# Optimization experiments

Hardware: AMD Instinct MI355X
Metric: run time of the kernel (lower is better)

The kernel has to match this reference:

```python
import jax, jax.numpy as jnp
import numpy as np

B, S, D = 2, 2048, 4096
H, KVH, HD = 32, 8, 128
THETA = 10000.0


def setup_inputs() -> dict:
    key = jax.random.key(0)
    k1, k2, k3 = jax.random.split(key, 3)
    hidden_states = jax.random.normal(k1, (B, S, D), jnp.float32)
    w_qkv = jax.random.normal(k2, ((KVH * 2 + H) * HD, D), jnp.float32) * 0.02
    w_dense = jax.random.normal(k3, (D, D), jnp.float32) * 0.02
    return {"hidden_states": hidden_states, "w_qkv": w_qkv, "w_dense": w_dense}


def _rope(x, pos):
    # x: [B, H, S, HD]; Falcon rotary embedding (rotate_half convention)
    inv_freq = 1.0 / (THETA ** (jnp.arange(0, HD, 2, dtype=jnp.float32) / HD))
    freqs = pos[:, None] * inv_freq[None, :]           # [S, HD/2]
    emb = jnp.concatenate([freqs, freqs], axis=-1)      # [S, HD]
    cos, sin = jnp.cos(emb), jnp.sin(emb)
    x1, x2 = x[..., : HD // 2], x[..., HD // 2 :]
    rot = jnp.concatenate([-x2, x1], axis=-1)
    return x * cos + rot * sin


def reference(hidden_states, w_qkv, w_dense):
    # fused QKV projection (FalconLinear, no bias)
    fused = jnp.einsum('bsd,ed->bse', hidden_states, w_qkv)  # [B,S,(2KVH+H)*HD]
    g = H // KVH  # query heads per kv head
    qkv = fused.reshape(B, S, KVH, g + 2, HD)
    q = qkv[:, :, :, :g]                        # [B,S,KVH,g,HD]
    k = jnp.broadcast_to(qkv[:, :, :, g:g + 1], q.shape)
    v = jnp.broadcast_to(qkv[:, :, :, g + 1:g + 2], q.shape)
    q, k, v = (t.reshape(B, S, H, HD).transpose(0, 2, 1, 3) for t in (q, k, v))
    pos = jnp.arange(S, dtype=jnp.float32)
    q = _rope(q, pos)
    k = _rope(k, pos)
    scores = jnp.einsum('bhqd,bhkd->bhqk', q, k) / jnp.sqrt(jnp.float32(HD))
    causal = jnp.tril(jnp.ones((S, S), dtype=bool))
    scores = jnp.where(causal, scores, jnp.float32(-1e9))
    attn = jax.nn.softmax(scores, axis=-1)
    out = jnp.einsum('bhqk,bhkd->bhqd', attn, v)
    out = out.transpose(0, 2, 1, 3).reshape(B, S, H * HD)   # merge heads
    return jnp.einsum('bsd,ed->bse', out, w_dense)
```

## Files before the change

kernel.cpp:

```cpp
#include <hip/hip_runtime.h>

#define B_   2
#define S_   2048
#define D_   4096
#define H_   32
#define KVH_ 8
#define HD_  128
#define NE_  6144

using f32x4  = __attribute__((ext_vector_type(4))) float;
using bf16x8 = __attribute__((ext_vector_type(8))) __bf16;

__device__ __forceinline__ unsigned short f2bf(float f) {
  union { float f; unsigned u; } v; v.f = f;
  unsigned r = v.u + 0x7FFFu + ((v.u >> 16) & 1u);
  return (unsigned short)(r >> 16);
}
__device__ __forceinline__ float bf2f(unsigned short h) {
  union { unsigned u; float f; } v; v.u = ((unsigned)h) << 16; return v.f;
}
__device__ __forceinline__ bf16x8 ld8(const unsigned short* p) {
  return *reinterpret_cast<const bf16x8*>(p);
}
__device__ __forceinline__ bf16x8 ld8b(const void* base, int byte_off) {
  return *reinterpret_cast<const bf16x8*>((const char*)base + byte_off);
}
__device__ __forceinline__ void cp16(const void* g, void* l) {
  __builtin_amdgcn_global_load_lds(
      (const __attribute__((address_space(1))) void*)g,
      (__attribute__((address_space(3))) void*)l, 16, 0, 0);
}

__global__ __launch_bounds__(256) void cvt_f32_bf16(
    const float* __restrict__ in, unsigned short* __restrict__ out, int n4)
{
  int i = blockIdx.x * 256 + threadIdx.x;
  if (i >= n4) return;
  f32x4 v = *reinterpret_cast<const f32x4*>(in + (size_t)i * 4);
  ushort4 o;
  o.x = f2bf(v[0]); o.y = f2bf(v[1]); o.z = f2bf(v[2]); o.w = f2bf(v[3]);
  *reinterpret_cast<ushort4*>(out + (size_t)i * 4) = o;
}

__global__ __launch_bounds__(256) void cvt2_f32_bf16(
    const float* __restrict__ s0, unsigned short* __restrict__ d0, int n0,
    const float* __restrict__ s1, unsigned short* __restrict__ d1, int n1)
{
  int i = blockIdx.x * 256 + threadIdx.x;
  const float* src; unsigned short* dst;
  if (i < n0) { src = s0; dst = d0; }
  else        { i -= n0; if (i >= n1) return; src = s1; dst = d1; }
  f32x4 v = *reinterpret_cast<const f32x4*>(src + (size_t)i * 4);
  ushort4 o;
  o.x = f2bf(v[0]); o.y = f2bf(v[1]); o.z = f2bf(v[2]); o.w = f2bf(v[3]);
  *reinterpret_cast<ushort4*>(dst + (size_t)i * 4) = o;
}

template <typename OutT, int NT>
__global__ __launch_bounds__(512, 2) void gemm256(
    const unsigned short* __restrict__ A,
    const unsigned short* __restrict__ Bw,
    OutT* __restrict__ C, int M, int N)
{
  constexpr int K  = 4096;
  constexpr int NI = (K / 64) / 2;
  constexpr int NB = NT / 64;
  constexpr int NN = NT / 64;
  constexpr int WN = NT / 4;
  constexpr int BBUF = NT * 128;
  __shared__ __align__(16) char lds[65536 + 2 * BBUF];

  const int tid  = threadIdx.x;
  const int lane = tid & 63;
  const int wave = tid >> 6;
  const int wr = wave >> 2;
  const int wc = wave & 3;
  const int lr = lane & 15;
  const int lk = (lane >> 4) * 8;

  int id  = blockIdx.y * gridDim.x + blockIdx.x;
  const int nwg = gridDim.x * gridDim.y;
  if ((nwg & 7) == 0) { const int q = nwg >> 3; id = (id & 7) * q + (id >> 3); }
  const int row0 = (id / gridDim.x) * 256;
  const int col0 = (id % gridDim.x) * NT;

  int rwA[2], csA[2], dbA[2];
#pragma unroll
  for (int j = 0; j < 2; ++j) {
    dbA[j] = j * 8192 + tid * 16;
    rwA[j] = dbA[j] >> 7;
    csA[j] = ((dbA[j] & 127) ^ ((rwA[j] & 7) << 4)) >> 1;
  }
  auto stA = [&](int buf, int h, int t) {
#pragma unroll
    for (int j = 0; j < 2; ++j)
      cp16(A + (size_t)(row0 + h * 128 + rwA[j]) * K + t * 64 + csA[j],
           lds + buf * 32768 + h * 16384 + dbA[j]);
  };
  const int dbB = tid * 16;
  const int rwB = dbB >> 7;
  const int csB = ((dbB & 127) ^ ((rwB & 7) << 4)) >> 1;
  auto stB = [&](int buf, int c, int t) {
    cp16(Bw + (size_t)(col0 + c * 64 + rwB) * K + t * 64 + csB,
         lds + 65536 + buf * BBUF + c * 8192 + dbB);
  };

  const int cb0 = ((0 + lk) << 1) ^ ((lr & 7) << 4);
  const int cb1 = ((32 + lk) << 1) ^ ((lr & 7) << 4);
  const int aRowB = (wr * 128 + lr) * 128;
  const int bRowB = (wc * WN + lr) * 128;

  f32x4 acc[8][NN];
#pragma unroll
  for (int m = 0; m < 8; ++m)
#pragma unroll
    for (int n = 0; n < NN; ++n) acc[m][n] = (f32x4){0.f, 0.f, 0.f, 0.f};
  bf16x8 bfr[NN][2];

#define FENCE asm volatile("" ::: "memory")
#define VMNB  do { if constexpr (NB == 4) asm volatile("s_waitcnt vmcnt(4)" ::: "memory"); \
                   else                   asm volatile("s_waitcnt vmcnt(3)" ::: "memory"); } while (0)
#define VM0   asm volatile("s_waitcnt vmcnt(0)" ::: "memory")

#define PHASE(p, buf, STAGE, WAIT)                                             \
  {                                                                            \
    if ((p) == 0) {                                                            \
      _Pragma("unroll")                                                        \
      for (int n = 0; n < NN; ++n) {                                           \
        bfr[n][0] = ld8b(lds, 65536 + (buf) * BBUF + bRowB + n * 2048 + cb0);  \
        bfr[n][1] = ld8b(lds, 65536 + (buf) * BBUF + bRowB + n * 2048 + cb1);  \
      }                                                                        \
    }                                                                          \
    bf16x8 a00 = ld8b(lds, (buf) * 32768 + aRowB + ((p) * 2 + 0) * 2048 + cb0);\
    bf16x8 a01 = ld8b(lds, (buf) * 32768 + aRowB + ((p) * 2 + 0) * 2048 + cb1);\
    bf16x8 a10 = ld8b(lds, (buf) * 32768 + aRowB + ((p) * 2 + 1) * 2048 + cb0);\
    bf16x8 a11 = ld8b(lds, (buf) * 32768 + aRowB + ((p) * 2 + 1) * 2048 + cb1);\
    STAGE;                                                                     \
    FENCE;                                                                     \
    __builtin_amdgcn_s_barrier();                                              \
    __builtin_amdgcn_s_setprio(1);                                             \
    _Pragma("unroll")                                                          \
    for (int n = 0; n < NN; ++n) {                                             \
      acc[(p)*2+0][n] = __builtin_amdgcn_mfma_f32_16x16x32_bf16(a00, bfr[n][0], acc[(p)*2+0][n], 0, 0, 0); \
      acc[(p)*2+0][n] = __builtin_amdgcn_mfma_f32_16x16x32_bf16(a01, bfr[n][1], acc[(p)*2+0][n], 0, 0, 0); \
      acc[(p)*2+1][n] = __builtin_amdgcn_mfma_f32_16x16x32_bf16(a10, bfr[n][0], acc[(p)*2+1][n], 0, 0, 0); \
      acc[(p)*2+1][n] = __builtin_amdgcn_mfma_f32_16x16x32_bf16(a11, bfr[n][1], acc[(p)*2+1][n], 0, 0, 0); \
    }                                                                          \
    __builtin_amdgcn_s_setprio(0);                                             \
    WAIT;                                                                      \
    FENCE;                                                                     \
    __builtin_amdgcn_s_barrier();                                              \
  }

#pragma unroll
  for (int c = 0; c < NB; ++c) stB(0, c, 0);
  stA(0, 0, 0); stA(0, 1, 0);
#pragma unroll
  for (int c = 0; c < NB; ++c) stB(1, c, 1);
  VMNB;
  FENCE;
  __builtin_amdgcn_s_barrier();

  for (int i = 0; i < NI; ++i) {
    const int t1  = 2 * i + 1;
    const int tn0 = 2 * i + 2;
    const int tn1 = 2 * i + 3;
    const bool pre = (i + 1 < NI);
    PHASE(0, 0, { stA(1, 0, t1); }, {});
    PHASE(1, 0, { stA(1, 1, t1); }, {});
    PHASE(2, 0, { if (pre) { stB(0, 0, tn0); stB(0, 1, tn0); } }, {});
    PHASE(3, 0, { if (pre) { _Pragma("unroll") for (int c = 2; c < NB; ++c) stB(0, c, tn0); } },
          { if (pre) { VMNB; } else { VM0; } });
    PHASE(0, 1, { if (pre) stA(0, 0, tn0); }, {});
    PHASE(1, 1, { if (pre) stA(0, 1, tn0); }, {});
    PHASE(2, 1, { if (pre) { stB(1, 0, tn1); stB(1, 1, tn1); } }, {});
    PHASE(3, 1, { if (pre) { _Pragma("unroll") for (int c = 2; c < NB; ++c) stB(1, c, tn1); } },
          { if (pre) { VMNB; } });
  }
#undef PHASE
#undef FENCE
#undef VMNB
#undef VM0

  const int orow = (lane >> 4) * 4;
#pragma unroll
  for (int m = 0; m < 8; ++m) {
    const int gr0 = row0 + wr * 128 + m * 16 + orow;
#pragma unroll
    for (int n = 0; n < NN; ++n) {
      const int gc = col0 + wc * WN + n * 16 + lr;
#pragma unroll
      for (int r = 0; r < 4; ++r) {
        float val = acc[m][n][r];
        if constexpr (sizeof(OutT) == 2)
          C[(size_t)(gr0 + r) * N + gc] = f2bf(val);
        else
          C[(size_t)(gr0 + r) * N + gc] = val;
      }
    }
  }
}

__global__ __launch_bounds__(256) void rope_scatter(
    const unsigned short* __restrict__ fused,
    unsigned short* __restrict__ Qr,
    unsigned short* __restrict__ Kr,
    unsigned short* __restrict__ Vt)
{
  int idx = blockIdx.x * 256 + threadIdx.x;
  int d = idx & 63;
  int t = idx >> 6;
  int e = t % 48;
  int bs = t / 48;
  int s = bs % S_;
  int b = bs / S_;
  int kvh = e / 6, j = e % 6;
  const unsigned short* src = fused + (size_t)bs * NE_ + e * 128;
  unsigned short u1 = src[d];
  unsigned short u2 = src[d + 64];
  if (j == 5) {
    size_t base = (size_t)(b * KVH_ + kvh) * HD_ * S_;
    Vt[base + (size_t)d * S_ + s]        = u1;
    Vt[base + (size_t)(d + 64) * S_ + s] = u2;
  } else {
    float x1 = bf2f(u1), x2 = bf2f(u2);
    float inv = __expf(-(float)d * (9.2103403719761836f / 64.0f));
    float ang = (float)s * inv;
    float sn, c;
    sincosf(ang, &sn, &c);
    float o1 = x1 * c - x2 * sn;
    float o2 = x2 * c + x1 * sn;
    unsigned short* dst;
    if (j == 4) dst = Kr + ((size_t)(b * KVH_ + kvh) * S_ + s) * HD_;
    else        dst = Qr + ((size_t)(b * H_ + kvh * 4 + j) * S_ + s) * HD_;
    dst[d]      = f2bf(o1);
    dst[d + 64] = f2bf(o2);
  }
}

__global__ __launch_bounds__(256) void attn_fwd(
    const unsigned short* __restrict__ Qr,
    const unsigned short* __restrict__ Kr,
    const unsigned short* __restrict__ Vt,
    unsigned short* __restrict__ O)
{
  __shared__ __align__(16) unsigned short Kld[2][64 * 128];
  __shared__ __align__(16) unsigned short Vld[2][128 * 64];
  __shared__ __align__(16) unsigned short Pld[4][16 * 64];

  const int tid  = threadIdx.x;
  const int lane = tid & 63;
  const int wave = tid >> 6;
  const int bx = blockIdx.x;
  const int h  = blockIdx.y;
  const int b  = blockIdx.z;
  const int kvh = h >> 2;
  const int lr = lane & 15;
  const int lk = (lane >> 4) * 8;
  const int orow = (lane >> 4) * 4;

  const float scale = 0.08838834764831845f;
  const unsigned short* Kb = Kr + (size_t)(b * KVH_ + kvh) * S_ * HD_;
  const unsigned short* Vb = Vt + (size_t)(b * KVH_ + kvh) * HD_ * S_;

  auto stage = [&](int buf, int kb) {
#pragma unroll
    for (int i = 0; i < 4; ++i) {
      const int db = i * 4096 + tid * 16;
      {
        const int row  = db >> 8;
        const int colb = (db & 255) ^ ((row & 7) << 4);
        cp16(Kb + (size_t)(kb * 64 + row) * HD_ + (colb >> 1),
             (char*)&Kld[buf][0] + i * 4096 + wave * 1024);
      }
      {
        const int row  = db >> 7;
        const int colb = (db & 127) ^ ((row & 7) << 4);
        cp16(Vb + (size_t)row * S_ + kb * 64 + (colb >> 1),
             (char*)&Vld[buf][0] + i * 4096 + wave * 1024);
      }
    }
  };

  for (int half = 0; half < 2; ++half) {
    const int qb = half ? (S_ / 64 - 1 - bx) : bx;

    const unsigned short* qbase =
        Qr + ((size_t)(b * H_ + h) * S_ + qb * 64 + wave * 16 + lr) * HD_;
    bf16x8 qf[4];
#pragma unroll
    for (int t = 0; t < 4; ++t) qf[t] = ld8(qbase + t * 32 + lk);

    f32x4 acc_o[8];
#pragma unroll
    for (int dt = 0; dt < 8; ++dt) acc_o[dt] = (f32x4){0.f, 0.f, 0.f, 0.f};
    float mrow[4], lrow[4];
#pragma unroll
    for (int r = 0; r < 4; ++r) { mrow[r] = -1e30f; lrow[r] = 0.f; }

    stage(0, 0);
    __syncthreads();

    for (int kb = 0; kb <= qb; ++kb) {
      const int cur = kb & 1;
      if (kb < qb) stage(cur ^ 1, kb + 1);

      const char* Kc = (const char*)&Kld[cur][0];
      const char* Vc = (const char*)&Vld[cur][0];

      f32x4 accs[4];
#pragma unroll
      for (int kt = 0; kt < 4; ++kt) accs[kt] = (f32x4){0.f, 0.f, 0.f, 0.f};
      __builtin_amdgcn_s_setprio(1);
#pragma unroll
      for (int t = 0; t < 4; ++t) {
#pragma unroll
        for (int kt = 0; kt < 4; ++kt) {
          const int krow = kt * 16 + lr;
          const int kbyte = ((krow << 8) + ((t * 32 + lk) << 1)) ^ ((krow & 7) << 4);
          bf16x8 kf = ld8b(Kc, kbyte);
          accs[kt] = __builtin_amdgcn_mfma_f32_16x16x32_bf16(qf[t], kf, accs[kt], 0, 0, 0);
        }
      }
      __builtin_amdgcn_s_setprio(0);

      const bool last = (kb == qb);
      float sv[4][4];
#pragma unroll
      for (int r = 0; r < 4; ++r) {
        const int qg = qb * 64 + wave * 16 + orow + r;
#pragma unroll
        for (int kt = 0; kt < 4; ++kt) {
          float v = accs[kt][r] * scale;
          int kg = kb * 64 + kt * 16 + lr;
          if (last && kg > qg) v = -1e30f;
          sv[r][kt] = v;
        }
      }

      float mnew[4], corr[4];
#pragma unroll
      for (int r = 0; r < 4; ++r) {
        float mx = fmaxf(fmaxf(sv[r][0], sv[r][1]), fmaxf(sv[r][2], sv[r][3]));
#pragma unroll
        for (int msk = 8; msk >= 1; msk >>= 1) mx = fmaxf(mx, __shfl_xor(mx, msk, 64));
        mnew[r] = fmaxf(mrow[r], mx);
        corr[r] = __expf(mrow[r] - mnew[r]);
        mrow[r] = mnew[r];
      }
#pragma unroll
      for (int r = 0; r < 4; ++r) {
        float su = 0.f;
#pragma unroll
        for (int kt = 0; kt < 4; ++kt) {
          float p = __expf(sv[r][kt] - mnew[r]);
          su += p;
          const int prow = orow + r;
          const int pbyte = ((prow << 7) + ((kt * 16 + lr) << 1)) ^ ((prow & 7) << 4);
          *(unsigned short*)((char*)&Pld[wave][0] + pbyte) = f2bf(p);
        }
#pragma unroll
        for (int msk = 8; msk >= 1; msk >>= 1) su += __shfl_xor(su, msk, 64);
        lrow[r] = lrow[r] * corr[r] + su;
      }
#pragma unroll
      for (int dt = 0; dt < 8; ++dt)
#pragma unroll
        for (int r = 0; r < 4; ++r) acc_o[dt][r] *= corr[r];

      asm volatile("" ::: "memory");

      __builtin_amdgcn_s_setprio(1);
#pragma unroll
      for (int kc = 0; kc < 2; ++kc) {
        const int pbyte = ((lr << 7) + ((kc * 32 + lk) << 1)) ^ ((lr & 7) << 4);
        bf16x8 pf = ld8b(&Pld[wave][0], pbyte);
#pragma unroll
        for (int dt = 0; dt < 8; ++dt) {
          const int vrow = dt * 16 + lr;
          const int vbyte = ((vrow << 7) + ((kc * 32 + lk) << 1)) ^ ((vrow & 7) << 4);
          bf16x8 vf = ld8b(Vc, vbyte);
          acc_o[dt] = __builtin_amdgcn_mfma_f32_16x16x32_bf16(pf, vf, acc_o[dt], 0, 0, 0);
        }
      }
      __builtin_amdgcn_s_setprio(0);

      __syncthreads();
    }

#pragma unroll
    for (int r = 0; r < 4; ++r) {
      float inv = 1.f / lrow[r];
      size_t rowoff =
          (size_t)(b * S_ + qb * 64 + wave * 16 + orow + r) * (H_ * HD_) + h * HD_;
#pragma unroll
      for (int dt = 0; dt < 8; ++dt)
        O[rowoff + dt * 16 + lr] = f2bf(acc_o[dt][r] * inv);
    }
  }
}

__global__ void fill_sentinel(float* __restrict__ O, int n) {
  int i = blockIdx.x * 256 + threadIdx.x;
  if (i < n) O[i] = 12345.0f;
}

extern "C" void kernel_launch(void* const* d_in, const int* in_sizes, int n_in,
                              void* d_out, int out_size, void* d_ws, size_t ws_size,
                              hipStream_t stream) {
  const float* hidden = (const float*)d_in[0];
  const float* wqkv   = (const float*)d_in[1];
  const float* wdense = (const float*)d_in[2];
  float* out = (float*)d_out;

  const size_t NEED = 134217728;
  if (ws_size < NEED) {
    fill_sentinel<<<dim3((out_size + 255) / 256), dim3(256), 0, stream>>>(out, out_size);
    return;
  }

  char* ws = (char*)d_ws;
  unsigned short* Hb    = (unsigned short*)(ws);
  unsigned short* Wqb   = (unsigned short*)(ws + 33554432);
  unsigned short* fused = (unsigned short*)(ws + 83886080);
  unsigned short* Qr    = (unsigned short*)(ws);
  unsigned short* Kr    = (unsigned short*)(ws + 33554432);
  unsigned short* Vt    = (unsigned short*)(ws + 41943040);
  unsigned short* Wdb   = (unsigned short*)(ws + 50331648);
  unsigned short* attn_out = (unsigned short*)(ws + 83886080);

  const int nH4 = B_ * S_ * D_ / 4;
  const int nQ4 = NE_ * D_ / 4;
  const int nD4 = D_ * D_ / 4;

  cvt2_f32_bf16<<<dim3((nH4 + nQ4 + 255) / 256), dim3(256), 0, stream>>>(
      hidden, Hb, nH4, wqkv, Wqb, nQ4);

  gemm256<unsigned short, 192><<<dim3(NE_ / 192, (B_ * S_) / 256), dim3(512), 0, stream>>>(
      Hb, Wqb, fused, B_ * S_, NE_);

  cvt_f32_bf16<<<dim3(nD4 / 256), dim3(256), 0, stream>>>(wdense, Wdb, nD4);

  rope_scatter<<<dim3((B_ * S_ * 48 * 64) / 256), dim3(256), 0, stream>>>(
      fused, Qr, Kr, Vt);

  attn_fwd<<<dim3(16, H_, B_), dim3(256), 0, stream>>>(Qr, Kr, Vt, attn_out);

  gemm256<float, 256><<<dim3(D_ / 256, (B_ * S_) / 256), dim3(512), 0, stream>>>(
      attn_out, Wdb, out, B_ * S_, D_);
}
```

Measured before the change: 560.4 us.

## Streamline attention softmax with exp2, prescaled Q, lazy rescale and deferred row sums

Folds the softmax scale and log2(e) into Q at load time so the inner loop runs exp2 directly on raw scores through a raw v_exp_f32. The running-max rescale is skipped whenever every row's new max stays within 8 of the stored max across the wave. The per-iteration row-sum shuffle reduction becomes a per-lane partial sum that is reduced once at the end. Together these cut VALU and cross-lane work in the softmax between the two MFMA phases. The cost is an extra bf16 rounding of the scaled Q and intermediate values up to 2^8 before normalisation, which could slightly change accuracy.

After: 527.4 us. 5.9% less time.

```diff
diff --git a/kernel.cpp b/kernel.cpp
--- a/kernel.cpp
+++ b/kernel.cpp
@@ -29,6 +29,9 @@
   __builtin_amdgcn_global_load_lds(
       (const __attribute__((address_space(1))) void*)g,
       (__attribute__((address_space(3))) void*)l, 16, 0, 0);
+}
+__device__ __forceinline__ float exp2a(float x) {
+  float r; asm("v_exp_f32 %0, %1" : "=v"(r) : "v"(x)); return r;
 }
 
 __global__ __launch_bounds__(256) void cvt_f32_bf16(
@@ -259,7 +262,7 @@
   const int lk = (lane >> 4) * 8;
   const int orow = (lane >> 4) * 4;
 
-  const float scale = 0.08838834764831845f;
+  const float SC2 = 0.08838834764831845f * 1.4426950408889634f;
   const unsigned short* Kb = Kr + (size_t)(b * KVH_ + kvh) * S_ * HD_;
   const unsigned short* Vb = Vt + (size_t)(b * KVH_ + kvh) * HD_ * S_;
 
@@ -289,14 +292,20 @@
         Qr + ((size_t)(b * H_ + h) * S_ + qb * 64 + wave * 16 + lr) * HD_;
     bf16x8 qf[4];
 #pragma unroll
-    for (int t = 0; t < 4; ++t) qf[t] = ld8(qbase + t * 32 + lk);
+    for (int t = 0; t < 4; ++t) {
+      union { bf16x8 v; unsigned short s[8]; } u;
+      u.v = ld8(qbase + t * 32 + lk);
+#pragma unroll
+      for (int j = 0; j < 8; ++j) u.s[j] = f2bf(bf2f(u.s[j]) * SC2);
+      qf[t] = u.v;
+    }
 
     f32x4 acc_o[8];
 #pragma unroll
     for (int dt = 0; dt < 8; ++dt) acc_o[dt] = (f32x4){0.f, 0.f, 0.f, 0.f};
-    float mrow[4], lrow[4];
-#pragma unroll
-    for (int r = 0; r < 4; ++r) { mrow[r] = -1e30f; lrow[r] = 0.f; }
+    float mrow[4], lpart[4];
+#pragma unroll
+    for (int r = 0; r < 4; ++r) { mrow[r] = -1e30f; lpart[r] = 0.f; }
 
     stage(0, 0);
     __syncthreads();
@@ -324,49 +333,51 @@
       }
       __builtin_amdgcn_s_setprio(0);
 
-      const bool last = (kb == qb);
-      float sv[4][4];
+      if (kb == qb) {
+#pragma unroll
+        for (int r = 0; r < 4; ++r) {
+          const int qg = wave * 16 + orow + r;
+#pragma unroll
+          for (int kt = 0; kt < 4; ++kt)
+            if (kt * 16 + lr > qg) accs[kt][r] = -1e30f;
+        }
+      }
+
+      float mx[4];
+#pragma unroll
+      for (int r = 0; r < 4; ++r)
+        mx[r] = fmaxf(fmaxf(accs[0][r], accs[1][r]), fmaxf(accs[2][r], accs[3][r]));
+      int ok = (mx[0] <= mrow[0] + 8.f) && (mx[1] <= mrow[1] + 8.f) &&
+               (mx[2] <= mrow[2] + 8.f) && (mx[3] <= mrow[3] + 8.f);
+      if (!__all(ok)) {
+        float corr[4];
+#pragma unroll
+        for (int r = 0; r < 4; ++r) {
+          float m = mx[r];
+#pragma unroll
+          for (int msk = 8; msk >= 1; msk >>= 1) m = fmaxf(m, __shfl_xor(m, msk, 64));
+          float mnew = fmaxf(mrow[r], m);
+          corr[r] = exp2a(mrow[r] - mnew);
+          mrow[r] = mnew;
+          lpart[r] *= corr[r];
+        }
+#pragma unroll
+        for (int dt = 0; dt < 8; ++dt)
+#pragma unroll
+          for (int r = 0; r < 4; ++r) acc_o[dt][r] *= corr[r];
+      }
+
 #pragma unroll
       for (int r = 0; r < 4; ++r) {
-        const int qg = qb * 64 + wave * 16 + orow + r;
+        const int prow = orow + r;
 #pragma unroll
         for (int kt = 0; kt < 4; ++kt) {
-          float v = accs[kt][r] * scale;
-          int kg = kb * 64 + kt * 16 + lr;
-          if (last && kg > qg) v = -1e30f;
-          sv[r][kt] = v;
+          float p = exp2a(accs[kt][r] - mrow[r]);
+          lpart[r] += p;
+          const int pbyte = ((prow << 7) + ((kt * 16 + lr) << 1)) ^ ((prow & 7) << 4);
+          *(__bf16*)((char*)&Pld[wave][0] + pbyte) = (__bf16)p;
         }
       }
-
-      float mnew[4], corr[4];
-#pragma unroll
-      for (int r = 0; r < 4; ++r) {
-        float mx = fmaxf(fmaxf(sv[r][0], sv[r][1]), fmaxf(sv[r][2], sv[r][3]));
-#pragma unroll
-        for (int msk = 8; msk >= 1; msk >>= 1) mx = fmaxf(mx, __shfl_xor(mx, msk, 64));
-        mnew[r] = fmaxf(mrow[r], mx);
-        corr[r] = __expf(mrow[r] - mnew[r]);
-        mrow[r] = mnew[r];
-      }
-#pragma unroll
-      for (int r = 0; r < 4; ++r) {
-        float su = 0.f;
-#pragma unroll
-        for (int kt = 0; kt < 4; ++kt) {
-          float p = __expf(sv[r][kt] - mnew[r]);
-          su += p;
-          const int prow = orow + r;
-          const int pbyte = ((prow << 7) + ((kt * 16 + lr) << 1)) ^ ((prow & 7) << 4);
-          *(unsigned short*)((char*)&Pld[wave][0] + pbyte) = f2bf(p);
-        }
-#pragma unroll
-        for (int msk = 8; msk >= 1; msk >>= 1) su += __shfl_xor(su, msk, 64);
-        lrow[r] = lrow[r] * corr[r] + su;
-      }
-#pragma unroll
-      for (int dt = 0; dt < 8; ++dt)
-#pragma unroll
-        for (int r = 0; r < 4; ++r) acc_o[dt][r] *= corr[r];
 
       asm volatile("" ::: "memory");
 
@@ -390,7 +401,10 @@
 
 #pragma unroll
     for (int r = 0; r < 4; ++r) {
-      float inv = 1.f / lrow[r];
+      float s = lpart[r];
+#pragma unroll
+      for (int msk = 8; msk >= 1; msk >>= 1) s += __shfl_xor(s, msk, 64);
+      float inv = 1.f / s;
       size_t rowoff =
           (size_t)(b * S_ + qb * 64 + wave * 16 + orow + r) * (H_ * HD_) + h * HD_;
 #pragma unroll
```
